# Optimization experiments

Hardware: AMD Instinct MI355X
Metric: run time of the kernel (lower is better)

## Reference

```python
import jax, jax.numpy as jnp
import numpy as np

B, S, Q, D = 8, 2048, 2048, 1024  # additive path requires S == Q


def setup_inputs() -> dict:
    key = jax.random.key(0)
    ks = jax.random.split(key, 5)
    def glorot(k, shape):
        fan_in, fan_out = shape[0], shape[1]
        limit = np.sqrt(6.0 / (fan_in + fan_out)).astype(np.float32)
        return jax.random.uniform(k, shape, jnp.float32, -limit, limit)
    return {
        "source": jax.random.normal(ks[0], (B, S, D), jnp.float32),
        "query": jax.random.normal(ks[1], (B, Q, D), jnp.float32),
        "kernel": glorot(ks[2], (S, Q)),
        "wk_kernel": glorot(ks[3], (D, Q)),
        "wq_kernel": glorot(ks[4], (S, D)),
    }


def reference(source, query, kernel, wk_kernel, wq_kernel):
    # query permuted to (B, D, Q) as in call()
    q_t = jnp.transpose(query, (0, 2, 1))
    # additive similarity: tanh(Wk . Source + Wq . Query) . kernel
    f_att = (jnp.einsum("bsd,dq->bsq", source, wk_kernel)
             + jnp.einsum("sd,bdq->bsq", wq_kernel, q_t))  # (B, S, Q)
    sim = jnp.einsum("bsq,qt->bst", jnp.tanh(f_att), kernel)  # (B, S, Q)
    sm = jax.nn.softmax(sim, axis=-1)  # softmax over last axis (Keras default)
    # sm_t = permute(sm, (0,2,1)); result = batch_dot(sm_t, Source)
    return jnp.einsum("bsq,bsd->bqd", sm, source)  # (B, Q, D)
```

## Files before the change

### kernel.cpp

```cpp
#include <hip/hip_runtime.h>
#include <hip/hip_bf16.h>
#include <stdint.h>

typedef unsigned short u16;

#define B_ 8
#define S_ 2048
#define Q_ 2048
#define D_ 1024
#define T_ 2048

typedef __attribute__((ext_vector_type(8))) short short8;
typedef __attribute__((ext_vector_type(16))) float f32x16;

__device__ __forceinline__ u16 f2b(float f) {
  union { float f; uint32_t u; } x; x.f = f;
  uint32_t r = x.u + 0x7fffu + ((x.u >> 16) & 1u);
  return (u16)(r >> 16);
}
__device__ __forceinline__ float b2f(u16 h) {
  union { uint32_t u; float f; } x; x.u = ((uint32_t)h) << 16;
  return x.f;
}
__device__ __forceinline__ float tanh_fast(float x) {
  return 1.0f - 2.0f / (__expf(2.0f * x) + 1.0f);
}
__device__ __forceinline__ void async16(const void* g, void* l) {
  __builtin_amdgcn_global_load_lds(
      (const __attribute__((address_space(1))) void*)g,
      (__attribute__((address_space(3))) void*)l, 16, 0, 0);
}

__global__ void cast_f32_bf16_k(const float* __restrict__ in, u16* __restrict__ out, int n4) {
  int i = blockIdx.x * 256 + threadIdx.x;
  if (i >= n4) return;
  float4 v = ((const float4*)in)[i];
  uint32_t lo = (uint32_t)f2b(v.x) | ((uint32_t)f2b(v.y) << 16);
  uint32_t hi = (uint32_t)f2b(v.z) | ((uint32_t)f2b(v.w) << 16);
  ((uint2*)out)[i] = make_uint2(lo, hi);
}

__global__ void transpose_f32_bf16_v(const float* __restrict__ in, u16* __restrict__ out,
                                     int R, int C) {
  __shared__ u16 t[64 * 72];
  int z = blockIdx.z;
  const float* pin = in + (size_t)z * R * C;
  u16* pout = out + (size_t)z * R * C;
  int c0 = blockIdx.x * 64, r0 = blockIdx.y * 64;
  int tid = threadIdx.x;
  int rr = tid >> 4, c4 = (tid & 15) * 4;
#pragma unroll
  for (int p = 0; p < 4; ++p) {
    int r = p * 16 + rr;
    float4 v = *(const float4*)&pin[(size_t)(r0 + r) * C + c0 + c4];
    t[(c4 + 0) * 72 + r] = f2b(v.x);
    t[(c4 + 1) * 72 + r] = f2b(v.y);
    t[(c4 + 2) * 72 + r] = f2b(v.z);
    t[(c4 + 3) * 72 + r] = f2b(v.w);
  }
  __syncthreads();
  int ct = tid >> 3, r8 = (tid & 7) * 8;
#pragma unroll
  for (int p = 0; p < 2; ++p) {
    int c = p * 32 + ct;
    uint2 lo = *(const uint2*)&t[c * 72 + r8];
    uint2 hi = *(const uint2*)&t[c * 72 + r8 + 4];
    *(uint4*)&pout[(size_t)(c0 + c) * R + r0 + r8] = make_uint4(lo.x, lo.y, hi.x, hi.y);
  }
}

__global__ void src_prep_v(const float* __restrict__ in, u16* __restrict__ outc,
                           u16* __restrict__ outT) {
  __shared__ u16 t[64 * 72];
  int z = blockIdx.z;
  const float* pin = in + (size_t)z * S_ * D_;
  u16* pc = outc + (size_t)z * S_ * D_;
  u16* pt = outT + (size_t)z * S_ * D_;
  int c0 = blockIdx.x * 64, r0 = blockIdx.y * 64;
  int tid = threadIdx.x;
  int rr = tid >> 4, c4 = (tid & 15) * 4;
#pragma unroll
  for (int p = 0; p < 4; ++p) {
    int r = p * 16 + rr;
    float4 v = *(const float4*)&pin[(size_t)(r0 + r) * D_ + c0 + c4];
    u16 b0 = f2b(v.x), b1 = f2b(v.y), b2 = f2b(v.z), b3 = f2b(v.w);
    uint2 pk;
    pk.x = (uint32_t)b0 | ((uint32_t)b1 << 16);
    pk.y = (uint32_t)b2 | ((uint32_t)b3 << 16);
    *(uint2*)&pc[(size_t)(r0 + r) * D_ + c0 + c4] = pk;
    t[(c4 + 0) * 72 + r] = b0;
    t[(c4 + 1) * 72 + r] = b1;
    t[(c4 + 2) * 72 + r] = b2;
    t[(c4 + 3) * 72 + r] = b3;
  }
  __syncthreads();
  int ct = tid >> 3, r8 = (tid & 7) * 8;
#pragma unroll
  for (int p = 0; p < 2; ++p) {
    int c = p * 32 + ct;
    uint2 lo = *(const uint2*)&t[c * 72 + r8];
    uint2 hi = *(const uint2*)&t[c * 72 + r8 + 4];
    *(uint4*)&pt[(size_t)(c0 + c) * S_ + r0 + r8] = make_uint4(lo.x, lo.y, hi.x, hi.y);
  }
}

__global__ void scale_srcT_k(u16* __restrict__ srcT, const float* __restrict__ l) {
  size_t i = (size_t)blockIdx.x * 256 + threadIdx.x;
  size_t e0 = i * 8;
  int s8 = (int)(e0 & (S_ - 1));
  int bb = (int)(e0 / ((size_t)D_ * S_));
  const float* lp = l + (size_t)bb * S_ + s8;
  float4 l0 = *(const float4*)lp;
  float4 l1 = *(const float4*)(lp + 4);
  uint4 raw = *(uint4*)&srcT[e0];
  uint32_t w[4] = {raw.x, raw.y, raw.z, raw.w};
  float li[8] = {l0.x, l0.y, l0.z, l0.w, l1.x, l1.y, l1.z, l1.w};
  uint32_t o[4];
#pragma unroll
  for (int k = 0; k < 4; ++k) {
    float a = b2f((u16)(w[k] & 0xffffu)) / li[2 * k];
    float b = b2f((u16)(w[k] >> 16)) / li[2 * k + 1];
    o[k] = (uint32_t)f2b(a) | ((uint32_t)f2b(b) << 16);
  }
  *(uint4*)&srcT[e0] = make_uint4(o[0], o[1], o[2], o[3]);
}

__global__ __launch_bounds__(512, 2) void gemm256_k(
    const u16* __restrict__ A1, long lda1, long bsA1,
    const u16* __restrict__ B1, long ldb1, long bsB1,
    const u16* __restrict__ A2, long lda2, long bsA2,
    const u16* __restrict__ B2, long ldb2, long bsB2,
    void* __restrict__ Cv, long ldc, long bsC,
    int K, int Srows, int nTerms, int mode, float* __restrict__ lsum) {
  __shared__ __align__(16) u16 lds[67584];

  const int tid = threadIdx.x;
  const int w = tid >> 6, lane = tid & 63;
  const int wr = w >> 2, wc = w & 3;
  const int l31 = lane & 31, hi = lane >> 5;

  const int gx = gridDim.x;
  const int nwg = gx * (int)gridDim.y;
  int lid = blockIdx.y * gx + blockIdx.x;
  if ((nwg & 7) == 0) lid = (lid & 7) * (nwg >> 3) + (lid >> 3);
  const int bn = lid % gx, bm = lid / gx;
  const int n0 = bn * 256, m0 = bm * 256;
  const int b = m0 / Srows;
  const int s0 = m0 - b * Srows;

  const int ktiles = K >> 6;
  const int ktlog = __ffs(ktiles) - 1;
  const int ktmask = ktiles - 1;
  const int NT = nTerms * ktiles;

  const u16* gA1 = A1 + (size_t)bsA1 * b + (size_t)s0 * lda1;
  const u16* gB1 = B1 + (size_t)bsB1 * b + (size_t)n0 * ldb1;
  const u16* gA2 = (nTerms > 1) ? (A2 + (size_t)bsA2 * b + (size_t)s0 * lda2) : gA1;
  const u16* gB2 = (nTerms > 1) ? (B2 + (size_t)bsB2 * b + (size_t)n0 * ldb2) : gB1;

  const int lrow = lane >> 3, lslot = lane & 7;
  const int gsl = (lslot ^ lrow) << 3;

  auto STG = [&](int tile, int isB, int half) {
    if (tile >= NT) return;
    const int term = tile >> ktlog;
    const int kt = (tile & ktmask) << 6;
    const u16* g = isB ? (term ? gB2 : gB1) : (term ? gA2 : gA1);
    const long ld = isB ? (term ? ldb2 : ldb1) : (term ? lda2 : lda1);
    u16* lb = lds + (tile & 1) * 33792 + isB * 16896;
#pragma unroll
    for (int is = 0; is < 2; ++is) {
      const int rh0 = is * 64 + w * 8;
      const int r0 = isB ? (half * 32 + (rh0 & 31) + ((rh0 >> 5) << 6))
                         : (half * 64 + (rh0 & 63) + ((rh0 >> 6) << 7));
      async16(g + (size_t)(r0 + lrow) * ld + kt + gsl, lb + (r0 >> 3) * 528);
    }
  };

  f32x16 acc[4][2];
#pragma unroll
  for (int x = 0; x < 4; ++x)
#pragma unroll
    for (int y = 0; y < 2; ++y)
#pragma unroll
      for (int r = 0; r < 16; ++r) acc[x][y][r] = 0.0f;

  u16* bufXA = lds;
  u16* bufXB = lds + 16896;
  u16* bufYA = lds + 33792;
  u16* bufYB = lds + 50688;

  const int aBase = (wr * 16 + (l31 >> 3)) * 528 + (l31 & 7) * 64;
  const int bBase = (wc * 8 + (l31 >> 3)) * 528 + (l31 & 7) * 64;
  int soff[4];
#pragma unroll
  for (int kk = 0; kk < 4; ++kk)
    soff[kk] = ((((kk << 1) | hi) ^ (l31 & 7)) << 3);

  short8 av[2][4], bv[4];

#define RD_AB(bufA, bufB, mh, nh)                                               \
  _Pragma("unroll") for (int kk = 0; kk < 4; ++kk) {                            \
    av[0][kk] = *(const short8*)&(bufA)[aBase + ((mh)*2 + 0) * 2112 + soff[kk]];\
    av[1][kk] = *(const short8*)&(bufA)[aBase + ((mh)*2 + 1) * 2112 + soff[kk]];\
    bv[kk]    = *(const short8*)&(bufB)[bBase + (nh)*2112 + soff[kk]];          \
  }
#define RD_A(bufA, mh)                                                          \
  _Pragma("unroll") for (int kk = 0; kk < 4; ++kk) {                            \
    av[0][kk] = *(const short8*)&(bufA)[aBase + ((mh)*2 + 0) * 2112 + soff[kk]];\
    av[1][kk] = *(const short8*)&(bufA)[aBase + ((mh)*2 + 1) * 2112 + soff[kk]];\
  }
#define RD_B(bufB, nh)                                                          \
  _Pragma("unroll") for (int kk = 0; kk < 4; ++kk)                              \
      bv[kk] = *(const short8*)&(bufB)[bBase + (nh)*2112 + soff[kk]];
#define BAR __builtin_amdgcn_s_barrier()
#define SB0 __builtin_amdgcn_sched_barrier(0)
#define LGKM0 asm volatile("s_waitcnt lgkmcnt(0)")
#define VMC4 asm volatile("s_waitcnt vmcnt(4)" ::: "memory")
#define VMC0 asm volatile("s_waitcnt vmcnt(0)" ::: "memory")
#define MFMA8(mh, nh)                                                         \
  __builtin_amdgcn_s_setprio(1);                                              \
  _Pragma("unroll") for (int kk = 0; kk < 4; ++kk)                            \
  _Pragma("unroll") for (int m = 0; m < 2; ++m)                               \
      acc[(mh)*2 + m][nh] = __builtin_amdgcn_mfma_f32_32x32x16_bf16(          \
          av[m][kk], bv[kk], acc[(mh)*2 + m][nh], 0, 0, 0);                   \
  __builtin_amdgcn_s_setprio(0)

  STG(0, 0, 0); STG(0, 1, 1); STG(0, 0, 1); STG(0, 1, 0);
  STG(1, 0, 0); STG(1, 1, 1);
  VMC4;
  BAR; SB0;

  const int niter = NT >> 1;
  for (int i = 0; i + 1 < niter; ++i) {
    const int u = 2 * i;
    RD_AB(bufXA, bufXB, 0, 0);
    STG(u + 1, 0, 1);
    BAR; LGKM0; SB0;
    MFMA8(0, 0);
    BAR;

    RD_B(bufXB, 1);
    STG(u + 1, 1, 0);
    BAR; LGKM0; SB0;
    MFMA8(0, 1);
    BAR;

    RD_A(bufXA, 1);
    STG(u + 2, 0, 0);
    BAR; LGKM0; SB0;
    MFMA8(1, 1);
    BAR;

    RD_B(bufXB, 0);
    STG(u + 2, 1, 1);
    BAR; LGKM0; SB0;
    MFMA8(1, 0);
    VMC4;
    BAR; SB0;

    RD_AB(bufYA, bufYB, 0, 0);
    STG(u + 2, 0, 1);
    BAR; LGKM0; SB0;
    MFMA8(0, 0);
    BAR;

    RD_B(bufYB, 1);
    STG(u + 2, 1, 0);
    BAR; LGKM0; SB0;
    MFMA8(0, 1);
    BAR;

    RD_A(bufYA, 1);
    STG(u + 3, 0, 0);
    BAR; LGKM0; SB0;
    MFMA8(1, 1);
    BAR;

    RD_B(bufYB, 0);
    STG(u + 3, 1, 1);
    BAR; LGKM0; SB0;
    MFMA8(1, 0);
    VMC4;
    BAR; SB0;
  }

  {
    const int u = NT - 2;
    RD_AB(bufXA, bufXB, 0, 0);
    STG(u + 1, 0, 1);
    BAR; LGKM0; SB0;
    MFMA8(0, 0);
    BAR;

    RD_B(bufXB, 1);
    STG(u + 1, 1, 0);
    BAR; LGKM0; SB0;
    MFMA8(0, 1);
    BAR;

    RD_A(bufXA, 1);
    BAR; LGKM0; SB0;
    MFMA8(1, 1);
    BAR;

    RD_B(bufXB, 0);
    BAR; LGKM0; SB0;
    MFMA8(1, 0);
    VMC0;
    BAR; SB0;

    RD_AB(bufYA, bufYB, 0, 0);
    BAR; LGKM0; SB0;
    MFMA8(0, 0);
    BAR;

    RD_B(bufYB, 1);
    BAR; LGKM0; SB0;
    MFMA8(0, 1);
    BAR;

    RD_A(bufYA, 1);
    BAR; LGKM0; SB0;
    MFMA8(1, 1);
    BAR;

    RD_B(bufYB, 0);
    BAR; LGKM0; SB0;
    MFMA8(1, 0);
  }

  if (mode == 3) {
#pragma unroll
    for (int mi = 0; mi < 4; ++mi)
#pragma unroll
      for (int ni = 0; ni < 2; ++ni)
#pragma unroll
        for (int r = 0; r < 16; ++r) acc[mi][ni][r] = __expf(acc[mi][ni][r]);
    float* lrowp = lsum + (size_t)b * Srows + s0;
#pragma unroll
    for (int mi = 0; mi < 4; ++mi)
#pragma unroll
      for (int r = 0; r < 16; ++r) {
        float pv = acc[mi][0][r] + acc[mi][1][r];
        pv += __shfl_xor(pv, 1);
        pv += __shfl_xor(pv, 2);
        pv += __shfl_xor(pv, 4);
        pv += __shfl_xor(pv, 8);
        pv += __shfl_xor(pv, 16);
        if (l31 == 0) {
          const int row = wr * 128 + mi * 32 + (r & 3) + 8 * (r >> 2) + 4 * hi;
          atomicAdd(&lrowp[row], pv);
        }
      }
    u16* gP = (u16*)Cv + (size_t)bsC * b + (size_t)n0 * ldc + s0;
    __syncthreads();
#pragma unroll
    for (int p = 0; p < 2; ++p) {
      if ((wc >> 1) == p) {
#pragma unroll
        for (int mi = 0; mi < 4; ++mi)
#pragma unroll
          for (int ni = 0; ni < 2; ++ni) {
            const int tc = (wc & 1) * 64 + ni * 32 + l31;
#pragma unroll
            for (int g2 = 0; g2 < 4; ++g2) {
              const int sr = wr * 128 + mi * 32 + g2 * 8 + hi * 4;
              u16 p0 = f2b(acc[mi][ni][g2 * 4 + 0]);
              u16 p1 = f2b(acc[mi][ni][g2 * 4 + 1]);
              u16 p2 = f2b(acc[mi][ni][g2 * 4 + 2]);
              u16 p3 = f2b(acc[mi][ni][g2 * 4 + 3]);
              uint2 pk;
              pk.x = (uint32_t)p0 | ((uint32_t)p1 << 16);
              pk.y = (uint32_t)p2 | ((uint32_t)p3 << 16);
              *(uint2*)&lds[tc * 268 + sr] = pk;
            }
          }
      }
      __syncthreads();
#pragma unroll
      for (int j = 0; j < 8; ++j) {
        const int idx = j * 512 + tid;
        const int tt = idx >> 5, s8 = (idx & 31) * 8;
        uint2 lo = *(const uint2*)&lds[tt * 268 + s8];
        uint2 h2 = *(const uint2*)&lds[tt * 268 + s8 + 4];
        *(uint4*)&gP[(size_t)(p * 128 + tt) * ldc + s8] =
            make_uint4(lo.x, lo.y, h2.x, h2.y);
      }
      __syncthreads();
    }
    return;
  }

  const size_t cb = (size_t)bsC * b + (size_t)s0 * ldc + n0;
  if (mode == 2) {
    float* C = (float*)Cv + cb;
#pragma unroll
    for (int mi = 0; mi < 4; ++mi)
#pragma unroll
      for (int ni = 0; ni < 2; ++ni) {
        const int col = wc * 64 + ni * 32 + l31;
#pragma unroll
        for (int r = 0; r < 16; ++r) {
          const int row = wr * 128 + mi * 32 + (r & 3) + 8 * (r >> 2) + 4 * hi;
          C[(size_t)row * ldc + col] = acc[mi][ni][r];
        }
      }
  } else {
    u16* C = (u16*)Cv + cb;
#pragma unroll
    for (int mi = 0; mi < 4; ++mi)
#pragma unroll
      for (int ni = 0; ni < 2; ++ni) {
        const int col = wc * 64 + ni * 32 + l31;
#pragma unroll
        for (int r = 0; r < 16; ++r) {
          const int row = wr * 128 + mi * 32 + (r & 3) + 8 * (r >> 2) + 4 * hi;
          float v = acc[mi][ni][r];
          if (mode == 0) v = tanh_fast(v);
          C[(size_t)row * ldc + col] = f2b(v);
        }
      }
  }
}

#undef RD_AB
#undef RD_A
#undef RD_B
#undef BAR
#undef SB0
#undef LGKM0
#undef VMC4
#undef VMC0
#undef MFMA8

extern "C" void kernel_launch(void* const* d_in, const int* in_sizes, int n_in,
                              void* d_out, int out_size, void* d_ws, size_t ws_size,
                              hipStream_t stream) {
  const float* src = (const float*)d_in[0];
  const float* qry = (const float*)d_in[1];
  const float* ker = (const float*)d_in[2];
  const float* wk  = (const float*)d_in[3];
  const float* wq  = (const float*)d_in[4];
  float* out = (float*)d_out;
  u16* ws = (u16*)d_ws;

  u16* srcb  = ws;
  u16* qryb  = srcb  + (size_t)B_ * S_ * D_;
  u16* wqb   = qryb  + (size_t)B_ * Q_ * D_;
  u16* wkT   = wqb   + (size_t)S_ * D_;
  u16* kerT  = wkT   + (size_t)D_ * Q_;
  u16* srcT  = kerT  + (size_t)Q_ * T_;
  u16* tanhT = srcT  + (size_t)B_ * D_ * S_;
  u16* PT    = tanhT + (size_t)B_ * S_ * Q_;
  float* l   = (float*)(PT + (size_t)B_ * T_ * S_);

  dim3 tb(256);

  cast_f32_bf16_k<<<(B_ * Q_ * D_) / 1024, 256, 0, stream>>>(qry, qryb, (B_ * Q_ * D_) / 4);
  cast_f32_bf16_k<<<(S_ * D_) / 1024, 256, 0, stream>>>(wq, wqb, (S_ * D_) / 4);
  transpose_f32_bf16_v<<<dim3(Q_ / 64, D_ / 64, 1), tb, 0, stream>>>(wk, wkT, D_, Q_);
  transpose_f32_bf16_v<<<dim3(T_ / 64, Q_ / 64, 1), tb, 0, stream>>>(ker, kerT, Q_, T_);
  src_prep_v<<<dim3(D_ / 64, S_ / 64, B_), tb, 0, stream>>>(src, srcb, srcT);
  hipMemsetAsync(l, 0, (size_t)B_ * S_ * sizeof(float), stream);

  gemm256_k<<<dim3(Q_ / 256, (B_ * S_) / 256), 512, 0, stream>>>(
      srcb, D_, (long)S_ * D_,
      wkT, D_, 0,
      wqb, D_, 0,
      qryb, D_, (long)Q_ * D_,
      tanhT, Q_, (long)S_ * Q_,
      D_, S_, 2, 0, nullptr);

  gemm256_k<<<dim3(T_ / 256, (B_ * S_) / 256), 512, 0, stream>>>(
      tanhT, Q_, (long)S_ * Q_,
      kerT, Q_, 0,
      nullptr, 0, 0, nullptr, 0, 0,
      PT, S_, (long)T_ * S_,
      Q_, S_, 1, 3, l);

  scale_srcT_k<<<(B_ * D_ * S_) / (256 * 8), 256, 0, stream>>>(srcT, l);

  gemm256_k<<<dim3(D_ / 256, (B_ * T_) / 256), 512, 0, stream>>>(
      PT, S_, (long)T_ * S_,
      srcT, S_, (long)D_ * S_,
      nullptr, 0, 0, nullptr, 0, 0,
      out, D_, (long)T_ * D_,
      S_, T_, 1, 2, nullptr);
}
```

Measured before the change: 654.7 us.

## Switch GEMM to 16x16x32 MFMA with unpadded XOR-swizzled LDS layout

Replaces the 32x32x16 bf16 MFMA tiling with 16x16x32 MFMA fragments (8x4 accumulators per wave). The LDS staging drops row padding for a dense 64-element row layout with an XOR swizzle applied both on the async global-to-LDS writes and on the fragment reads. The epilogues, row-sum reduction and P transpose store are remapped to the new accumulator layout. This changes the LDS bank-conflict pattern and instruction mix, and risks more conflicts or more MFMA issue overhead if the swizzle is imperfect.

```diff
diff --git a/kernel.cpp b/kernel.cpp
--- a/kernel.cpp
+++ b/kernel.cpp
@@ -11,7 +11,7 @@
 #define T_ 2048
 
 typedef __attribute__((ext_vector_type(8))) short short8;
-typedef __attribute__((ext_vector_type(16))) float f32x16;
+typedef __attribute__((ext_vector_type(4))) float f32x4;
 
 __device__ __forceinline__ u16 f2b(float f) {
   union { float f; uint32_t u; } x; x.f = f;
@@ -132,12 +132,12 @@
     const u16* __restrict__ B2, long ldb2, long bsB2,
     void* __restrict__ Cv, long ldc, long bsC,
     int K, int Srows, int nTerms, int mode, float* __restrict__ lsum) {
-  __shared__ __align__(16) u16 lds[67584];
+  __shared__ __align__(16) u16 lds[65536];
 
   const int tid = threadIdx.x;
   const int w = tid >> 6, lane = tid & 63;
   const int wr = w >> 2, wc = w & 3;
-  const int l31 = lane & 31, hi = lane >> 5;
+  const int l15 = lane & 15, lhi4 = lane >> 4;
 
   const int gx = gridDim.x;
   const int nwg = gx * (int)gridDim.y;
@@ -158,8 +158,8 @@
   const u16* gA2 = (nTerms > 1) ? (A2 + (size_t)bsA2 * b + (size_t)s0 * lda2) : gA1;
   const u16* gB2 = (nTerms > 1) ? (B2 + (size_t)bsB2 * b + (size_t)n0 * ldb2) : gB1;
 
-  const int lrow = lane >> 3, lslot = lane & 7;
-  const int gsl = (lslot ^ lrow) << 3;
+  const int lrow = lane >> 3;
+  const int gk = ((lane & 7) ^ ((lane >> 5) << 1)) * 8;
 
   auto STG = [&](int tile, int isB, int half) {
     if (tile >= NT) return;
@@ -167,63 +167,55 @@
     const int kt = (tile & ktmask) << 6;
     const u16* g = isB ? (term ? gB2 : gB1) : (term ? gA2 : gA1);
     const long ld = isB ? (term ? ldb2 : ldb1) : (term ? lda2 : lda1);
-    u16* lb = lds + (tile & 1) * 33792 + isB * 16896;
+    u16* lb = lds + (tile & 1) * 32768 + isB * 16384;
 #pragma unroll
     for (int is = 0; is < 2; ++is) {
-      const int rh0 = is * 64 + w * 8;
-      const int r0 = isB ? (half * 32 + (rh0 & 31) + ((rh0 >> 5) << 6))
-                         : (half * 64 + (rh0 & 63) + ((rh0 >> 6) << 7));
-      async16(g + (size_t)(r0 + lrow) * ld + kt + gsl, lb + (r0 >> 3) * 528);
+      const int ci = is * 8 + w;
+      const int r0 = isB ? ((ci >> 2) * 64 + half * 32 + (ci & 3) * 8)
+                         : (is * 128 + half * 64 + w * 8);
+      async16(g + (size_t)(r0 + lrow) * ld + kt + gk, lb + r0 * 64);
     }
   };
 
-  f32x16 acc[4][2];
-#pragma unroll
-  for (int x = 0; x < 4; ++x)
-#pragma unroll
-    for (int y = 0; y < 2; ++y)
-#pragma unroll
-      for (int r = 0; r < 16; ++r) acc[x][y][r] = 0.0f;
+  f32x4 acc[8][4];
+#pragma unroll
+  for (int x = 0; x < 8; ++x)
+#pragma unroll
+    for (int y = 0; y < 4; ++y)
+#pragma unroll
+      for (int r = 0; r < 4; ++r) acc[x][y][r] = 0.0f;
 
   u16* bufXA = lds;
-  u16* bufXB = lds + 16896;
-  u16* bufYA = lds + 33792;
-  u16* bufYB = lds + 50688;
-
-  const int aBase = (wr * 16 + (l31 >> 3)) * 528 + (l31 & 7) * 64;
-  const int bBase = (wc * 8 + (l31 >> 3)) * 528 + (l31 & 7) * 64;
-  int soff[4];
-#pragma unroll
-  for (int kk = 0; kk < 4; ++kk)
-    soff[kk] = ((((kk << 1) | hi) ^ (l31 & 7)) << 3);
-
-  short8 av[2][4], bv[4];
-
-#define RD_AB(bufA, bufB, mh, nh)                                               \
-  _Pragma("unroll") for (int kk = 0; kk < 4; ++kk) {                            \
-    av[0][kk] = *(const short8*)&(bufA)[aBase + ((mh)*2 + 0) * 2112 + soff[kk]];\
-    av[1][kk] = *(const short8*)&(bufA)[aBase + ((mh)*2 + 1) * 2112 + soff[kk]];\
-    bv[kk]    = *(const short8*)&(bufB)[bBase + (nh)*2112 + soff[kk]];          \
-  }
-#define RD_A(bufA, mh)                                                          \
-  _Pragma("unroll") for (int kk = 0; kk < 4; ++kk) {                            \
-    av[0][kk] = *(const short8*)&(bufA)[aBase + ((mh)*2 + 0) * 2112 + soff[kk]];\
-    av[1][kk] = *(const short8*)&(bufA)[aBase + ((mh)*2 + 1) * 2112 + soff[kk]];\
-  }
-#define RD_B(bufB, nh)                                                          \
-  _Pragma("unroll") for (int kk = 0; kk < 4; ++kk)                              \
-      bv[kk] = *(const short8*)&(bufB)[bBase + (nh)*2112 + soff[kk]];
+  u16* bufXB = lds + 16384;
+  u16* bufYA = lds + 32768;
+  u16* bufYB = lds + 49152;
+
+  const int rsx = ((l15 >> 2) & 1) << 4;
+  const int aBase = (((wr * 128 + l15) * 64) + lhi4 * 8) ^ rsx;
+  const int bBase = (((wc * 64 + l15) * 64) + lhi4 * 8) ^ rsx;
+
+  short8 av[4][2], bv[2][2];
+
+#define RD_A(bufA, mh)                                                         \
+  _Pragma("unroll") for (int kk = 0; kk < 2; ++kk)                             \
+  _Pragma("unroll") for (int fr = 0; fr < 4; ++fr)                             \
+      av[fr][kk] = *(const short8*)&(bufA)[aBase + (mh)*4096 + fr * 1024 + kk * 32];
+#define RD_B(bufB, bp)                                                         \
+  _Pragma("unroll") for (int kk = 0; kk < 2; ++kk)                             \
+  _Pragma("unroll") for (int fc = 0; fc < 2; ++fc)                             \
+      bv[fc][kk] = *(const short8*)&(bufB)[bBase + (bp)*2048 + fc * 1024 + kk * 32];
 #define BAR __builtin_amdgcn_s_barrier()
 #define SB0 __builtin_amdgcn_sched_barrier(0)
 #define LGKM0 asm volatile("s_waitcnt lgkmcnt(0)")
 #define VMC4 asm volatile("s_waitcnt vmcnt(4)" ::: "memory")
 #define VMC0 asm volatile("s_waitcnt vmcnt(0)" ::: "memory")
-#define MFMA8(mh, nh)                                                         \
-  __builtin_amdgcn_s_setprio(1);                                              \
-  _Pragma("unroll") for (int kk = 0; kk < 4; ++kk)                            \
-  _Pragma("unroll") for (int m = 0; m < 2; ++m)                               \
-      acc[(mh)*2 + m][nh] = __builtin_amdgcn_mfma_f32_32x32x16_bf16(          \
-          av[m][kk], bv[kk], acc[(mh)*2 + m][nh], 0, 0, 0);                   \
+#define MFMA16(mh, bp)                                                         \
+  __builtin_amdgcn_s_setprio(1);                                               \
+  _Pragma("unroll") for (int kk = 0; kk < 2; ++kk)                             \
+  _Pragma("unroll") for (int fr = 0; fr < 4; ++fr)                             \
+  _Pragma("unroll") for (int fc = 0; fc < 2; ++fc)                             \
+      acc[(mh)*4 + fr][(bp)*2 + fc] = __builtin_amdgcn_mfma_f32_16x16x32_bf16( \
+          av[fr][kk], bv[fc][kk], acc[(mh)*4 + fr][(bp)*2 + fc], 0, 0, 0);     \
   __builtin_amdgcn_s_setprio(0)
 
   STG(0, 0, 0); STG(0, 1, 1); STG(0, 0, 1); STG(0, 1, 0);
@@ -234,122 +226,120 @@
   const int niter = NT >> 1;
   for (int i = 0; i + 1 < niter; ++i) {
     const int u = 2 * i;
-    RD_AB(bufXA, bufXB, 0, 0);
+    RD_A(bufXA, 0); RD_B(bufXB, 0);
     STG(u + 1, 0, 1);
     BAR; LGKM0; SB0;
-    MFMA8(0, 0);
+    MFMA16(0, 0);
     BAR;
 
     RD_B(bufXB, 1);
     STG(u + 1, 1, 0);
     BAR; LGKM0; SB0;
-    MFMA8(0, 1);
+    MFMA16(0, 1);
     BAR;
 
     RD_A(bufXA, 1);
     STG(u + 2, 0, 0);
     BAR; LGKM0; SB0;
-    MFMA8(1, 1);
+    MFMA16(1, 1);
     BAR;
 
     RD_B(bufXB, 0);
     STG(u + 2, 1, 1);
     BAR; LGKM0; SB0;
-    MFMA8(1, 0);
+    MFMA16(1, 0);
     VMC4;
     BAR; SB0;
 
-    RD_AB(bufYA, bufYB, 0, 0);
+    RD_A(bufYA, 0); RD_B(bufYB, 0);
     STG(u + 2, 0, 1);
     BAR; LGKM0; SB0;
-    MFMA8(0, 0);
+    MFMA16(0, 0);
     BAR;
 
     RD_B(bufYB, 1);
     STG(u + 2, 1, 0);
     BAR; LGKM0; SB0;
-    MFMA8(0, 1);
+    MFMA16(0, 1);
     BAR;
 
     RD_A(bufYA, 1);
     STG(u + 3, 0, 0);
     BAR; LGKM0; SB0;
-    MFMA8(1, 1);
+    MFMA16(1, 1);
     BAR;
 
     RD_B(bufYB, 0);
     STG(u + 3, 1, 1);
     BAR; LGKM0; SB0;
-    MFMA8(1, 0);
+    MFMA16(1, 0);
     VMC4;
     BAR; SB0;
   }
 
   {
-    const int u = NT - 2;
-    RD_AB(bufXA, bufXB, 0, 0);
-    STG(u + 1, 0, 1);
-    BAR; LGKM0; SB0;
-    MFMA8(0, 0);
+    RD_A(bufXA, 0); RD_B(bufXB, 0);
+    STG(NT - 1, 0, 1);
+    BAR; LGKM0; SB0;
+    MFMA16(0, 0);
     BAR;
 
     RD_B(bufXB, 1);
-    STG(u + 1, 1, 0);
-    BAR; LGKM0; SB0;
-    MFMA8(0, 1);
+    STG(NT - 1, 1, 0);
+    BAR; LGKM0; SB0;
+    MFMA16(0, 1);
     BAR;
 
     RD_A(bufXA, 1);
     BAR; LGKM0; SB0;
-    MFMA8(1, 1);
+    MFMA16(1, 1);
     BAR;
 
     RD_B(bufXB, 0);
     BAR; LGKM0; SB0;
-    MFMA8(1, 0);
+    MFMA16(1, 0);
     VMC0;
     BAR; SB0;
 
-    RD_AB(bufYA, bufYB, 0, 0);
-    BAR; LGKM0; SB0;
-    MFMA8(0, 0);
+    RD_A(bufYA, 0); RD_B(bufYB, 0);
+    BAR; LGKM0; SB0;
+    MFMA16(0, 0);
     BAR;
 
     RD_B(bufYB, 1);
     BAR; LGKM0; SB0;
-    MFMA8(0, 1);
+    MFMA16(0, 1);
     BAR;
 
     RD_A(bufYA, 1);
     BAR; LGKM0; SB0;
-    MFMA8(1, 1);
+    MFMA16(1, 1);
     BAR;
 
     RD_B(bufYB, 0);
     BAR; LGKM0; SB0;
-    MFMA8(1, 0);
+    MFMA16(1, 0);
   }
 
   if (mode == 3) {
 #pragma unroll
-    for (int mi = 0; mi < 4; ++mi)
-#pragma unroll
-      for (int ni = 0; ni < 2; ++ni)
-#pragma unroll
-        for (int r = 0; r < 16; ++r) acc[mi][ni][r] = __expf(acc[mi][ni][r]);
+    for (int fr = 0; fr < 8; ++fr)
+#pragma unroll
+      for (int fc = 0; fc < 4; ++fc)
+#pragma unroll
+        for (int r = 0; r < 4; ++r) acc[fr][fc][r] = __expf(acc[fr][fc][r]);
     float* lrowp = lsum + (size_t)b * Srows + s0;
 #pragma unroll
-    for (int mi = 0; mi < 4; ++mi)
-#pragma unroll
-      for (int r = 0; r < 16; ++r) {
-        float pv = acc[mi][0][r] + acc[mi][1][r];
+    for (int fr = 0; fr < 8; ++fr)
+#pragma unroll
+      for (int r = 0; r < 4; ++r) {
+        float pv = acc[fr][0][r] + acc[fr][1][r] + acc[fr][2][r] + acc[fr][3][r];
         pv += __shfl_xor(pv, 1);
         pv += __shfl_xor(pv, 2);
         pv += __shfl_xor(pv, 4);
         pv += __shfl_xor(pv, 8);
-        pv += __shfl_xor(pv, 16);
-        if (l31 == 0) {
-          const int row = wr * 128 + mi * 32 + (r & 3) + 8 * (r >> 2) + 4 * hi;
+        if (l15 == 0) {
+          const int row = wr * 128 + fr * 16 + lhi4 * 4 + r;
           atomicAdd(&lrowp[row], pv);
         }
       }
@@ -359,22 +349,19 @@
     for (int p = 0; p < 2; ++p) {
       if ((wc >> 1) == p) {
 #pragma unroll
-        for (int mi = 0; mi < 4; ++mi)
-#pragma unroll
-          for (int ni = 0; ni < 2; ++ni) {
-            const int tc = (wc & 1) * 64 + ni * 32 + l31;
-#pragma unroll
-            for (int g2 = 0; g2 < 4; ++g2) {
-              const int sr = wr * 128 + mi * 32 + g2 * 8 + hi * 4;
-              u16 p0 = f2b(acc[mi][ni][g2 * 4 + 0]);
-              u16 p1 = f2b(acc[mi][ni][g2 * 4 + 1]);
-              u16 p2 = f2b(acc[mi][ni][g2 * 4 + 2]);
-              u16 p3 = f2b(acc[mi][ni][g2 * 4 + 3]);
-              uint2 pk;
-              pk.x = (uint32_t)p0 | ((uint32_t)p1 << 16);
-              pk.y = (uint32_t)p2 | ((uint32_t)p3 << 16);
-              *(uint2*)&lds[tc * 268 + sr] = pk;
-            }
+        for (int fr = 0; fr < 8; ++fr)
+#pragma unroll
+          for (int fc = 0; fc < 4; ++fc) {
+            const int tc = (wc & 1) * 64 + fc * 16 + l15;
+            const int sl = wr * 128 + fr * 16 + lhi4 * 4;
+            u16 p0 = f2b(acc[fr][fc][0]);
+            u16 p1 = f2b(acc[fr][fc][1]);
+            u16 p2 = f2b(acc[fr][fc][2]);
+            u16 p3 = f2b(acc[fr][fc][3]);
+            uint2 pk;
+            pk.x = (uint32_t)p0 | ((uint32_t)p1 << 16);
+            pk.y = (uint32_t)p2 | ((uint32_t)p3 << 16);
+            *(uint2*)&lds[tc * 268 + sl] = pk;
           }
       }
       __syncthreads();
@@ -396,27 +383,27 @@
   if (mode == 2) {
     float* C = (float*)Cv + cb;
 #pragma unroll
-    for (int mi = 0; mi < 4; ++mi)
-#pragma unroll
-      for (int ni = 0; ni < 2; ++ni) {
-        const int col = wc * 64 + ni * 32 + l31;
-#pragma unroll
-        for (int r = 0; r < 16; ++r) {
-          const int row = wr * 128 + mi * 32 + (r & 3) + 8 * (r >> 2) + 4 * hi;
-          C[(size_t)row * ldc + col] = acc[mi][ni][r];
+    for (int fr = 0; fr < 8; ++fr)
+#pragma unroll
+      for (int fc = 0; fc < 4; ++fc) {
+        const int col = wc * 64 + fc * 16 + l15;
+#pragma unroll
+        for (int r = 0; r < 4; ++r) {
+          const int row = wr * 128 + fr * 16 + lhi4 * 4 + r;
+          C[(size_t)row * ldc + col] = acc[fr][fc][r];
         }
       }
   } else {
     u16* C = (u16*)Cv + cb;
 #pragma unroll
-    for (int mi = 0; mi < 4; ++mi)
-#pragma unroll
-      for (int ni = 0; ni < 2; ++ni) {
-        const int col = wc * 64 + ni * 32 + l31;
-#pragma unroll
-        for (int r = 0; r < 16; ++r) {
-          const int row = wr * 128 + mi * 32 + (r & 3) + 8 * (r >> 2) + 4 * hi;
-          float v = acc[mi][ni][r];
+    for (int fr = 0; fr < 8; ++fr)
+#pragma unroll
+      for (int fc = 0; fc < 4; ++fc) {
+        const int col = wc * 64 + fc * 16 + l15;
+#pragma unroll
+        for (int r = 0; r < 4; ++r) {
+          const int row = wr * 128 + fr * 16 + lhi4 * 4 + r;
+          float v = acc[fr][fc][r];
           if (mode == 0) v = tanh_fast(v);
           C[(size_t)row * ldc + col] = f2b(v);
         }
@@ -424,7 +411,6 @@
   }
 }
 
-#undef RD_AB
 #undef RD_A
 #undef RD_B
 #undef BAR
@@ -432,7 +418,7 @@
 #undef LGKM0
 #undef VMC4
 #undef VMC0
-#undef MFMA8
+#undef MFMA16
 
 extern "C" void kernel_launch(void* const* d_in, const int* in_sizes, int n_in,
                               void* d_out, int out_size, void* d_ws, size_t ws_size,
```

Result: faster. 602.9 us (-7.9%).
